# Kernel optimization log

Hardware: AMD Instinct MI355X
Metric: run time of the kernel (lower is better)

The kernel has to match this reference:

```python
import jax, jax.numpy as jnp
import numpy as np

N_NODES = 100000
N_EDGES = 1600000
IN_DIM, HID_DIM, OUT_DIM = 64, 64, 16


def setup_inputs() -> dict:
    key = jax.random.key(0)
    k1, k2, k3, k4 = jax.random.split(key, 4)
    x = jax.random.normal(k1, (N_NODES, IN_DIM), dtype=jnp.float32)
    edge_index = jax.random.randint(k2, (2, N_EDGES), 0, N_NODES, dtype=jnp.int64)
    W1 = jax.random.normal(k3, (IN_DIM, HID_DIM), dtype=jnp.float32) * (1.0 / np.sqrt(IN_DIM))
    b1 = jnp.zeros((HID_DIM,), dtype=jnp.float32)
    W2 = jax.random.normal(k4, (HID_DIM, OUT_DIM), dtype=jnp.float32) * (1.0 / np.sqrt(HID_DIM))
    b2 = jnp.zeros((OUT_DIM,), dtype=jnp.float32)
    return {"x": x, "edge_index": edge_index, "W1": W1, "b1": b1, "W2": W2, "b2": b2}


def gcn_conv(x, src, dst, W, b, num_nodes):
    """GCNConv: h = D^{-1/2} (A+I) D^{-1/2} (x W) + b, edge-list form with self-loops already appended."""
    # symmetric degree normalization (degree counted at destination, incl. self-loops)
    deg = jax.ops.segment_sum(jnp.ones_like(dst, dtype=x.dtype), dst, num_segments=num_nodes)
    dinv = jnp.where(deg > 0, jax.lax.rsqrt(deg), 0.0)
    norm = dinv[src] * dinv[dst]                      # [E+N]
    h = x @ W                                         # [N, H] project first (fewer flops on edges)
    msg = h[src] * norm[:, None]                      # gather + scale, [E+N, H]
    out = jax.ops.segment_sum(msg, dst, num_segments=num_nodes)  # scatter-add
    return out + b


def reference(x, edge_index, W1, b1, W2, b2):
    num_nodes = x.shape[0]
    loop = jnp.arange(num_nodes, dtype=edge_index.dtype)
    src = jnp.concatenate([edge_index[0], loop])      # add self-loops once, reuse for both layers
    dst = jnp.concatenate([edge_index[1], loop])
    h = gcn_conv(x, src, dst, W1, b1, num_nodes)
    h = jax.nn.relu(h)
    # F.dropout(training=self.training): eval mode -> identity
    out = gcn_conv(h, src, dst, W2, b2, num_nodes)
    return out
```

## Files before the change

kernel.cpp:

```cpp
#include <hip/hip_runtime.h>

constexpr int N_NODES = 100000;
constexpr int F1 = 64;
constexpr int F2 = 16;
constexpr int SH = 7;
constexpr int NPB = 128;
constexpr int NBINS = (N_NODES + NPB - 1) / NPB;
constexpr int CAPB = 2560;
constexpr int TILE = 4096;

static __device__ __forceinline__ unsigned short f2bf(float f) {
    unsigned int u = __float_as_uint(f);
    unsigned int r = (u + 0x7fffu + ((u >> 16) & 1u)) >> 16;
    return (unsigned short)r;
}
static __device__ __forceinline__ float bf2f(unsigned short b) {
    return __uint_as_float(((unsigned int)b) << 16);
}
static __device__ __forceinline__ float lo16(unsigned int u) { return __uint_as_float(u << 16); }
static __device__ __forceinline__ float hi16(unsigned int u) { return __uint_as_float(u & 0xFFFF0000u); }

__global__ __launch_bounds__(256) void k_bin(const int* __restrict__ src,
                                             const int* __restrict__ dst, int E,
                                             unsigned int* __restrict__ gcnt,
                                             unsigned int* __restrict__ entries) {
    __shared__ unsigned int cnt[NBINS];
    __shared__ unsigned int cur[NBINS];
    int tid = threadIdx.x;
    int base = blockIdx.x * TILE;
    int end = min(base + TILE, E);
    for (int i = tid; i < NBINS; i += 256) cnt[i] = 0;
    __syncthreads();
    for (int e = base + tid; e < end; e += 256) atomicAdd(&cnt[dst[e] >> SH], 1u);
    __syncthreads();
    for (int i = tid; i < NBINS; i += 256) {
        unsigned int c = cnt[i];
        cur[i] = (unsigned int)i * CAPB + (c ? atomicAdd(&gcnt[i], c) : 0u);
    }
    __syncthreads();
    for (int e = base + tid; e < end; e += 256) {
        int d = dst[e];
        int s = src[e];
        int bb = d >> SH;
        unsigned int p = atomicAdd(&cur[bb], 1u);
        if (p - (unsigned int)bb * CAPB < CAPB)
            entries[p] = (unsigned int)s | ((unsigned int)(d & (NPB - 1)) << 17);
    }
}

__global__ __launch_bounds__(256) void k_csr(const unsigned int* __restrict__ gcnt,
                                             const unsigned int* __restrict__ entries,
                                             uint2* __restrict__ nrange,
                                             unsigned int* __restrict__ sorted,
                                             float* __restrict__ dinv) {
    __shared__ unsigned int ncnt[NPB];
    __shared__ unsigned int noff[NPB + 1];
    __shared__ unsigned int cur[NPB];
    int tid = threadIdx.x;
    int b = blockIdx.x;
    unsigned int cntE = gcnt[b]; if (cntE > CAPB) cntE = CAPB;
    unsigned int base = (unsigned int)b * CAPB;
    if (tid < NPB) ncnt[tid] = 0;
    __syncthreads();
    for (unsigned int e = tid; e < cntE; e += 256)
        atomicAdd(&ncnt[entries[base + e] >> 17], 1u);
    __syncthreads();
    if (tid < NPB) cur[tid] = ncnt[tid];
    __syncthreads();
    for (int ofs = 1; ofs < NPB; ofs <<= 1) {
        unsigned int v = (tid < NPB && tid >= ofs) ? cur[tid - ofs] : 0u;
        __syncthreads();
        if (tid < NPB) cur[tid] += v;
        __syncthreads();
    }
    if (tid < NPB) noff[tid + 1] = cur[tid];
    if (tid == 0) noff[0] = 0;
    __syncthreads();
    if (tid < NPB) {
        int node = b * NPB + tid;
        if (node < N_NODES) {
            dinv[node] = rsqrtf((float)(ncnt[tid] + 1u));
            nrange[node] = make_uint2(base + noff[tid], base + noff[tid + 1]);
        }
        cur[tid] = noff[tid];
    }
    __syncthreads();
    for (unsigned int e = tid; e < cntE; e += 256) {
        unsigned int v = entries[base + e];
        unsigned int p = atomicAdd(&cur[v >> 17], 1u);
        sorted[base + p] = v & 0x1FFFFu;
    }
}

__global__ __launch_bounds__(256) void k_xw1(const float* __restrict__ x,
                                             const float* __restrict__ W,
                                             const float* __restrict__ dinv,
                                             unsigned short* __restrict__ hs) {
    constexpr int XS = 68;
    __shared__ float Ws[64 * 64];
    __shared__ float xs[64 * XS];
    int tid = threadIdx.x;
    int r0 = blockIdx.x * 64;
    for (int i = tid; i < 1024; i += 256) {
        int k = i >> 4, c4 = (i & 15) << 2;
        *(float4*)&Ws[k * 64 + c4] = *(const float4*)&W[k * 64 + c4];
    }
    for (int i = tid; i < 1024; i += 256) {
        int rr = i >> 4, c4 = (i & 15) << 2;
        int r = r0 + rr;
        float4 v = make_float4(0.f, 0.f, 0.f, 0.f);
        if (r < N_NODES) v = *(const float4*)&x[(size_t)r * 64 + c4];
        *(float4*)&xs[rr * XS + c4] = v;
    }
    __syncthreads();
    int tx = tid & 15, ty = tid >> 4;
    int c0 = tx << 2, rb = ty << 2;
    float acc[4][4] = {};
#pragma unroll 8
    for (int k = 0; k < 64; ++k) {
        float4 w = *(float4*)&Ws[k * 64 + c0];
        float x0 = xs[(rb + 0) * XS + k];
        float x1 = xs[(rb + 1) * XS + k];
        float x2 = xs[(rb + 2) * XS + k];
        float x3 = xs[(rb + 3) * XS + k];
        acc[0][0] += x0 * w.x; acc[0][1] += x0 * w.y; acc[0][2] += x0 * w.z; acc[0][3] += x0 * w.w;
        acc[1][0] += x1 * w.x; acc[1][1] += x1 * w.y; acc[1][2] += x1 * w.z; acc[1][3] += x1 * w.w;
        acc[2][0] += x2 * w.x; acc[2][1] += x2 * w.y; acc[2][2] += x2 * w.z; acc[2][3] += x2 * w.w;
        acc[3][0] += x3 * w.x; acc[3][1] += x3 * w.y; acc[3][2] += x3 * w.z; acc[3][3] += x3 * w.w;
    }
#pragma unroll
    for (int i = 0; i < 4; ++i) {
        int r = r0 + rb + i;
        if (r >= N_NODES) break;
        float dv = dinv[r];
        ushort4 p;
        p.x = f2bf(acc[i][0] * dv);
        p.y = f2bf(acc[i][1] * dv);
        p.z = f2bf(acc[i][2] * dv);
        p.w = f2bf(acc[i][3] * dv);
        *(ushort4*)&hs[(size_t)r * 64 + c0] = p;
    }
}

__global__ __launch_bounds__(256) void k_agg1f(const uint2* __restrict__ nrange,
                                               const unsigned int* __restrict__ sorted,
                                               const unsigned short* __restrict__ hs,
                                               const float* __restrict__ dinv,
                                               unsigned short* __restrict__ out1) {
    int gw = (blockIdx.x * 256 + threadIdx.x) >> 6;
    if (gw >= N_NODES) return;
    int lane = threadIdx.x & 63;
    int half = lane >> 5, t = lane & 31;
    const unsigned int* hs32 = (const unsigned int*)hs;
    uint2 rg = nrange[gw];
    float a0 = 0.f, a1 = 0.f;
    unsigned int j = rg.x + (unsigned)half, e = rg.y;
    for (; j + 6 < e; j += 8) {
        unsigned int s0 = sorted[j], s1 = sorted[j + 2], s2 = sorted[j + 4], s3 = sorted[j + 6];
        unsigned int u0 = hs32[(size_t)s0 * 32 + t];
        unsigned int u1 = hs32[(size_t)s1 * 32 + t];
        unsigned int u2 = hs32[(size_t)s2 * 32 + t];
        unsigned int u3 = hs32[(size_t)s3 * 32 + t];
        a0 += (lo16(u0) + lo16(u1)) + (lo16(u2) + lo16(u3));
        a1 += (hi16(u0) + hi16(u1)) + (hi16(u2) + hi16(u3));
    }
    for (; j < e; j += 2) {
        unsigned int u = hs32[(size_t)sorted[j] * 32 + t];
        a0 += lo16(u);
        a1 += hi16(u);
    }
    a0 += __shfl_xor(a0, 32);
    a1 += __shfl_xor(a1, 32);
    if (half == 0) {
        unsigned int u = hs32[(size_t)gw * 32 + t];
        a0 += lo16(u);
        a1 += hi16(u);
        float dv = dinv[gw];
        unsigned int w = (unsigned)f2bf(a0 * dv) | ((unsigned)f2bf(a1 * dv) << 16);
        ((unsigned int*)out1)[(size_t)gw * 32 + t] = w;
    }
}

__global__ __launch_bounds__(256) void k_xw2(const unsigned short* __restrict__ out1,
                                             const float* __restrict__ b1,
                                             const float* __restrict__ W2,
                                             const float* __restrict__ dinv,
                                             unsigned short* __restrict__ h2s) {
    constexpr int RS = 66;
    __shared__ float Ws[64 * 16];
    __shared__ float rs[128 * RS];
    __shared__ float b1s[64];
    int tid = threadIdx.x;
    int r0 = blockIdx.x * 128;
    if (tid < 64) b1s[tid] = b1[tid];
    for (int i = tid; i < 256; i += 256)
        *(float4*)&Ws[i * 4] = *(const float4*)&W2[i * 4];
    __syncthreads();
    for (int i = tid; i < 2048; i += 256) {
        int rr = i >> 4, c4 = (i & 15) << 2;
        int r = r0 + rr;
        float v0 = 0.f, v1 = 0.f, v2 = 0.f, v3 = 0.f;
        if (r < N_NODES) {
            ushort4 u = *(const ushort4*)&out1[(size_t)r * 64 + c4];
            v0 = fmaxf(bf2f(u.x) + b1s[c4 + 0], 0.f);
            v1 = fmaxf(bf2f(u.y) + b1s[c4 + 1], 0.f);
            v2 = fmaxf(bf2f(u.z) + b1s[c4 + 2], 0.f);
            v3 = fmaxf(bf2f(u.w) + b1s[c4 + 3], 0.f);
        }
        float* pp = &rs[rr * RS + c4];
        pp[0] = v0; pp[1] = v1; pp[2] = v2; pp[3] = v3;
    }
    __syncthreads();
    int tx = tid & 3, ty = tid >> 2;
    int c0 = tx << 2, rb = ty << 1;
    float acc[2][4] = {};
#pragma unroll 8
    for (int k = 0; k < 64; ++k) {
        float4 w = *(float4*)&Ws[k * 16 + c0];
        float x0 = rs[(rb + 0) * RS + k];
        float x1 = rs[(rb + 1) * RS + k];
        acc[0][0] += x0 * w.x; acc[0][1] += x0 * w.y; acc[0][2] += x0 * w.z; acc[0][3] += x0 * w.w;
        acc[1][0] += x1 * w.x; acc[1][1] += x1 * w.y; acc[1][2] += x1 * w.z; acc[1][3] += x1 * w.w;
    }
#pragma unroll
    for (int i = 0; i < 2; ++i) {
        int r = r0 + rb + i;
        if (r >= N_NODES) break;
        float dv = dinv[r];
        ushort4 p;
        p.x = f2bf(acc[i][0] * dv);
        p.y = f2bf(acc[i][1] * dv);
        p.z = f2bf(acc[i][2] * dv);
        p.w = f2bf(acc[i][3] * dv);
        *(ushort4*)&h2s[(size_t)r * 16 + c0] = p;
    }
}

__global__ __launch_bounds__(256) void k_agg2f(const uint2* __restrict__ nrange,
                                               const unsigned int* __restrict__ sorted,
                                               const unsigned short* __restrict__ h2s,
                                               const float* __restrict__ dinv,
                                               const float* __restrict__ b2,
                                               float* __restrict__ out) {
    int gw = (blockIdx.x * 256 + threadIdx.x) >> 6;
    if (gw >= N_NODES) return;
    int lane = threadIdx.x & 63;
    int slot = lane >> 3, t = lane & 7;
    const unsigned int* h232 = (const unsigned int*)h2s;
    uint2 rg = nrange[gw];
    float a0 = 0.f, a1 = 0.f;
    unsigned int j = rg.x, e = rg.y;
    for (; j + 16 <= e; j += 16) {
        unsigned int sA = sorted[j + slot];
        unsigned int sB = sorted[j + 8 + slot];
        unsigned int uA = h232[(size_t)sA * 8 + t];
        unsigned int uB = h232[(size_t)sB * 8 + t];
        a0 += lo16(uA) + lo16(uB);
        a1 += hi16(uA) + hi16(uB);
    }
    for (; j < e; j += 8) {
        unsigned int i1 = j + (unsigned)slot;
        if (i1 < e) {
            unsigned int u = h232[(size_t)sorted[i1] * 8 + t];
            a0 += lo16(u);
            a1 += hi16(u);
        }
    }
    a0 += __shfl_xor(a0, 8);
    a1 += __shfl_xor(a1, 8);
    a0 += __shfl_xor(a0, 16);
    a1 += __shfl_xor(a1, 16);
    a0 += __shfl_xor(a0, 32);
    a1 += __shfl_xor(a1, 32);
    if (slot == 0) {
        unsigned int u = h232[(size_t)gw * 8 + t];
        a0 += lo16(u);
        a1 += hi16(u);
        float dv = dinv[gw];
        float2 o;
        o.x = a0 * dv + b2[2 * t];
        o.y = a1 * dv + b2[2 * t + 1];
        *(float2*)&out[(size_t)gw * 16 + 2 * t] = o;
    }
}

static inline size_t align256(size_t x) { return (x + 255) & ~size_t(255); }

extern "C" void kernel_launch(void* const* d_in, const int* in_sizes, int n_in,
                              void* d_out, int out_size, void* d_ws, size_t ws_size,
                              hipStream_t stream) {
    const float* x  = (const float*)d_in[0];
    const int* edge = (const int*)d_in[1];
    const float* W1 = (const float*)d_in[2];
    const float* b1 = (const float*)d_in[3];
    const float* W2 = (const float*)d_in[4];
    const float* b2 = (const float*)d_in[5];
    float* out = (float*)d_out;

    const int E = in_sizes[1] / 2;
    const int* src = edge;
    const int* dst = edge + E;

    char* ws = (char*)d_ws;
    size_t o = 0;
    unsigned int* gcnt    = (unsigned int*)(ws + o); o += align256((size_t)NBINS * 4);
    float* dinv           = (float*)(ws + o);        o += align256((size_t)N_NODES * 4);
    unsigned int* entries = (unsigned int*)(ws + o); o += align256((size_t)NBINS * CAPB * 4);
    unsigned int* sorted  = (unsigned int*)(ws + o); o += align256((size_t)NBINS * CAPB * 4);
    uint2* nrange         = (uint2*)(ws + o);        o += align256((size_t)N_NODES * 8);
    unsigned short* hs    = (unsigned short*)(ws + o); o += align256((size_t)N_NODES * F1 * 2);
    unsigned short* out1  = (unsigned short*)(ws + o); o += align256((size_t)N_NODES * F1 * 2);
    unsigned short* h2s   = (unsigned short*)(ws + o); o += align256((size_t)N_NODES * F2 * 2);

    hipMemsetAsync(gcnt, 0, (size_t)NBINS * 4, stream);

    k_bin<<<(E + TILE - 1) / TILE, 256, 0, stream>>>(src, dst, E, gcnt, entries);
    k_csr<<<NBINS, 256, 0, stream>>>(gcnt, entries, nrange, sorted, dinv);

    k_xw1<<<(N_NODES + 63) / 64, 256, 0, stream>>>(x, W1, dinv, hs);
    {
        long long waves = (long long)N_NODES;
        int blocks = (int)((waves * 64 + 255) / 256);
        k_agg1f<<<blocks, 256, 0, stream>>>(nrange, sorted, hs, dinv, out1);
    }

    k_xw2<<<(N_NODES + 127) / 128, 256, 0, stream>>>(out1, b1, W2, dinv, h2s);
    {
        long long waves = (long long)N_NODES;
        int blocks = (int)((waves * 64 + 255) / 256);
        k_agg2f<<<blocks, 256, 0, stream>>>(nrange, sorted, h2s, dinv, b2, out);
    }
}
```

Before: 163.8 us.

## Fold self-loops into CSR and use cooperative index loads in aggregation

```diff
diff --git a/kernel.cpp b/kernel.cpp
--- a/kernel.cpp
+++ b/kernel.cpp
@@ -7,7 +7,7 @@
 constexpr int NPB = 128;
 constexpr int NBINS = (N_NODES + NPB - 1) / NPB;
 constexpr int CAPB = 2560;
-constexpr int TILE = 4096;
+constexpr int TILE = 8192;
 
 static __device__ __forceinline__ unsigned short f2bf(float f) {
     unsigned int u = __float_as_uint(f);
@@ -28,10 +28,13 @@
     __shared__ unsigned int cur[NBINS];
     int tid = threadIdx.x;
     int base = blockIdx.x * TILE;
-    int end = min(base + TILE, E);
+    int end = min(base + TILE, E + N_NODES);
     for (int i = tid; i < NBINS; i += 256) cnt[i] = 0;
     __syncthreads();
-    for (int e = base + tid; e < end; e += 256) atomicAdd(&cnt[dst[e] >> SH], 1u);
+    for (int e = base + tid; e < end; e += 256) {
+        int d = (e < E) ? dst[e] : (e - E);
+        atomicAdd(&cnt[d >> SH], 1u);
+    }
     __syncthreads();
     for (int i = tid; i < NBINS; i += 256) {
         unsigned int c = cnt[i];
@@ -39,8 +42,9 @@
     }
     __syncthreads();
     for (int e = base + tid; e < end; e += 256) {
-        int d = dst[e];
-        int s = src[e];
+        int d, s;
+        if (e < E) { d = dst[e]; s = src[e]; }
+        else       { d = e - E;  s = d; }
         int bb = d >> SH;
         unsigned int p = atomicAdd(&cur[bb], 1u);
         if (p - (unsigned int)bb * CAPB < CAPB)
@@ -79,7 +83,7 @@
     if (tid < NPB) {
         int node = b * NPB + tid;
         if (node < N_NODES) {
-            dinv[node] = rsqrtf((float)(ncnt[tid] + 1u));
+            dinv[node] = rsqrtf((float)max(ncnt[tid], 1u));
             nrange[node] = make_uint2(base + noff[tid], base + noff[tid + 1]);
         }
         cur[tid] = noff[tid];
@@ -150,34 +154,35 @@
     int gw = (blockIdx.x * 256 + threadIdx.x) >> 6;
     if (gw >= N_NODES) return;
     int lane = threadIdx.x & 63;
-    int half = lane >> 5, t = lane & 31;
-    const unsigned int* hs32 = (const unsigned int*)hs;
+    int slot = lane >> 4, t = lane & 15;
+    const uint2* hs8 = (const uint2*)hs;
     uint2 rg = nrange[gw];
-    float a0 = 0.f, a1 = 0.f;
-    unsigned int j = rg.x + (unsigned)half, e = rg.y;
-    for (; j + 6 < e; j += 8) {
-        unsigned int s0 = sorted[j], s1 = sorted[j + 2], s2 = sorted[j + 4], s3 = sorted[j + 6];
-        unsigned int u0 = hs32[(size_t)s0 * 32 + t];
-        unsigned int u1 = hs32[(size_t)s1 * 32 + t];
-        unsigned int u2 = hs32[(size_t)s2 * 32 + t];
-        unsigned int u3 = hs32[(size_t)s3 * 32 + t];
-        a0 += (lo16(u0) + lo16(u1)) + (lo16(u2) + lo16(u3));
-        a1 += (hi16(u0) + hi16(u1)) + (hi16(u2) + hi16(u3));
-    }
-    for (; j < e; j += 2) {
-        unsigned int u = hs32[(size_t)sorted[j] * 32 + t];
-        a0 += lo16(u);
-        a1 += hi16(u);
-    }
-    a0 += __shfl_xor(a0, 32);
-    a1 += __shfl_xor(a1, 32);
-    if (half == 0) {
-        unsigned int u = hs32[(size_t)gw * 32 + t];
-        a0 += lo16(u);
-        a1 += hi16(u);
+    float a0 = 0.f, a1 = 0.f, a2 = 0.f, a3 = 0.f;
+    for (unsigned int j = rg.x; j < rg.y; j += 64) {
+        unsigned int cnt = rg.y - j; if (cnt > 64u) cnt = 64u;
+        unsigned int idx = (unsigned)lane < cnt ? sorted[j + lane] : 0u;
+        unsigned int rounds = (cnt + 3u) >> 2;
+#pragma unroll 4
+        for (unsigned int r = 0; r < rounds; ++r) {
+            unsigned int sl = (r << 2) + (unsigned)slot;
+            unsigned int myidx = (unsigned int)__shfl((int)idx, (int)sl);
+            if (sl < cnt) {
+                uint2 u = hs8[(size_t)myidx * 16 + t];
+                a0 += lo16(u.x); a1 += hi16(u.x);
+                a2 += lo16(u.y); a3 += hi16(u.y);
+            }
+        }
+    }
+    a0 += __shfl_xor(a0, 16); a1 += __shfl_xor(a1, 16);
+    a2 += __shfl_xor(a2, 16); a3 += __shfl_xor(a3, 16);
+    a0 += __shfl_xor(a0, 32); a1 += __shfl_xor(a1, 32);
+    a2 += __shfl_xor(a2, 32); a3 += __shfl_xor(a3, 32);
+    if (slot == 0) {
         float dv = dinv[gw];
-        unsigned int w = (unsigned)f2bf(a0 * dv) | ((unsigned)f2bf(a1 * dv) << 16);
-        ((unsigned int*)out1)[(size_t)gw * 32 + t] = w;
+        uint2 w;
+        w.x = (unsigned)f2bf(a0 * dv) | ((unsigned)f2bf(a1 * dv) << 16);
+        w.y = (unsigned)f2bf(a2 * dv) | ((unsigned)f2bf(a3 * dv) << 16);
+        ((uint2*)out1)[(size_t)gw * 16 + t] = w;
     }
 }
 
@@ -249,33 +254,25 @@
     const unsigned int* h232 = (const unsigned int*)h2s;
     uint2 rg = nrange[gw];
     float a0 = 0.f, a1 = 0.f;
-    unsigned int j = rg.x, e = rg.y;
-    for (; j + 16 <= e; j += 16) {
-        unsigned int sA = sorted[j + slot];
-        unsigned int sB = sorted[j + 8 + slot];
-        unsigned int uA = h232[(size_t)sA * 8 + t];
-        unsigned int uB = h232[(size_t)sB * 8 + t];
-        a0 += lo16(uA) + lo16(uB);
-        a1 += hi16(uA) + hi16(uB);
-    }
-    for (; j < e; j += 8) {
-        unsigned int i1 = j + (unsigned)slot;
-        if (i1 < e) {
-            unsigned int u = h232[(size_t)sorted[i1] * 8 + t];
-            a0 += lo16(u);
-            a1 += hi16(u);
+    for (unsigned int j = rg.x; j < rg.y; j += 64) {
+        unsigned int cnt = rg.y - j; if (cnt > 64u) cnt = 64u;
+        unsigned int idx = (unsigned)lane < cnt ? sorted[j + lane] : 0u;
+        unsigned int rounds = (cnt + 7u) >> 3;
+#pragma unroll 4
+        for (unsigned int r = 0; r < rounds; ++r) {
+            unsigned int sl = (r << 3) + (unsigned)slot;
+            unsigned int myidx = (unsigned int)__shfl((int)idx, (int)sl);
+            if (sl < cnt) {
+                unsigned int u = h232[(size_t)myidx * 8 + t];
+                a0 += lo16(u);
+                a1 += hi16(u);
+            }
         }
     }
-    a0 += __shfl_xor(a0, 8);
-    a1 += __shfl_xor(a1, 8);
-    a0 += __shfl_xor(a0, 16);
-    a1 += __shfl_xor(a1, 16);
-    a0 += __shfl_xor(a0, 32);
-    a1 += __shfl_xor(a1, 32);
+    a0 += __shfl_xor(a0, 8);  a1 += __shfl_xor(a1, 8);
+    a0 += __shfl_xor(a0, 16); a1 += __shfl_xor(a1, 16);
+    a0 += __shfl_xor(a0, 32); a1 += __shfl_xor(a1, 32);
     if (slot == 0) {
-        unsigned int u = h232[(size_t)gw * 8 + t];
-        a0 += lo16(u);
-        a1 += hi16(u);
         float dv = dinv[gw];
         float2 o;
         o.x = a0 * dv + b2[2 * t];
@@ -314,20 +311,19 @@
 
     hipMemsetAsync(gcnt, 0, (size_t)NBINS * 4, stream);
 
-    k_bin<<<(E + TILE - 1) / TILE, 256, 0, stream>>>(src, dst, E, gcnt, entries);
+    int nbinblocks = (E + N_NODES + TILE - 1) / TILE;
+    k_bin<<<nbinblocks, 256, 0, stream>>>(src, dst, E, gcnt, entries);
     k_csr<<<NBINS, 256, 0, stream>>>(gcnt, entries, nrange, sorted, dinv);
 
     k_xw1<<<(N_NODES + 63) / 64, 256, 0, stream>>>(x, W1, dinv, hs);
     {
-        long long waves = (long long)N_NODES;
-        int blocks = (int)((waves * 64 + 255) / 256);
+        int blocks = (int)(((long long)N_NODES * 64 + 255) / 256);
         k_agg1f<<<blocks, 256, 0, stream>>>(nrange, sorted, hs, dinv, out1);
     }
 
     k_xw2<<<(N_NODES + 127) / 128, 256, 0, stream>>>(out1, b1, W2, dinv, h2s);
     {
-        long long waves = (long long)N_NODES;
-        int blocks = (int)((waves * 64 + 255) / 256);
+        int blocks = (int)(((long long)N_NODES * 64 + 255) / 256);
         k_agg2f<<<blocks, 256, 0, stream>>>(nrange, sorted, h2s, dinv, b2, out);
     }
 }
```

New measurement: 165.0 us. Within noise of the previous version (+0.7%).
